# Optimization experiments

Measured on AMD Instinct MI355X. Metric: run time of the kernel, lower is better.

The kernel has to match this reference:

```python
import jax, jax.numpy as jnp
import numpy as np
from jax import lax


def _conv1d(x, w, b, stride, pad):
    # x: [N, 1, L], w: [1, 1, K]
    y = lax.conv_general_dilated(x, w, (stride,), [(pad, pad)],
                                 dimension_numbers=('NCH', 'OIH', 'NCH'))
    return y + b[None, :, None]


def _maxpool1d(x, k, stride, pad):
    # torch MaxPool1d semantics: pad with -inf, window max
    return lax.reduce_window(x, -jnp.inf, lax.max,
                             (1, 1, k), (1, 1, stride),
                             ((0, 0), (0, 0), (pad, pad)))


def setup_inputs() -> dict:
    key = jax.random.key(0)
    ks = jax.random.split(key, 14)
    bs, n, T = 64, 1024, 1200
    return {
        'input':   jax.random.normal(ks[0], (bs, n, T), jnp.float32),
        'conv1_w': jax.random.normal(ks[1], (1, 1, 10), jnp.float32) * 0.3,
        'conv1_b': jax.random.normal(ks[2], (1,), jnp.float32) * 0.1,
        'conv2_w': jax.random.normal(ks[3], (1, 1, 3), jnp.float32) * 0.5,
        'conv2_b': jax.random.normal(ks[4], (1,), jnp.float32) * 0.1,
        'conv3_w': jax.random.normal(ks[5], (1, 1, 4), jnp.float32) * 0.5,
        'conv3_b': jax.random.normal(ks[6], (1,), jnp.float32) * 0.1,
        'gcn1_w':  jax.random.normal(ks[7], (30, 30), jnp.float32) * 0.18,
        'gcn1_b':  jax.random.normal(ks[8], (30,), jnp.float32) * 0.1,
        'gcn2_w':  jax.random.normal(ks[9], (4, 4), jnp.float32) * 0.5,
        'gcn2_b':  jax.random.normal(ks[10], (4,), jnp.float32) * 0.1,
        'cls_w':   jax.random.normal(ks[11], (3, n), jnp.float32) * 0.03,
        'cls_b':   jax.random.normal(ks[12], (3,), jnp.float32) * 0.1,
    }


def reference(input, conv1_w, conv1_b, conv2_w, conv2_b, conv3_w, conv3_b,
              gcn1_w, gcn1_b, gcn2_w, gcn2_b, cls_w, cls_b):
    bs, n, T = input.shape
    # Per-node 1-channel conv chain: fold nodes into the batch dim (replaces
    # the original Python loop over num_nodes issuing tiny Conv1d launches).
    x = input.reshape(bs * n, 1, T)
    h = jax.nn.relu(_conv1d(x, conv1_w, conv1_b, 8, 1))   # L: 1200 -> 150
    h = jax.nn.relu(_maxpool1d(h, 5, 5, 0))               # 150 -> 30
    # NOTE: original applies gcn1 to t_layer_out[2] here, but overwrites an
    # already-consumed list entry -> output is DEAD w.r.t. the final result.
    # (GCNConv over the all-ones adjacency == mean over nodes @ W.T + b.)
    h = jax.nn.relu(_conv1d(h, conv2_w, conv2_b, 3, 0))   # 30 -> 10
    h = jax.nn.relu(_maxpool1d(h, 3, 3, 1))               # 10 -> 4
    # Same dead-code situation for gcn2 on t_layer_out[4].
    h = jax.nn.relu(_conv1d(h, conv3_w, conv3_b, 1, 0))   # 4 -> 1
    feat = h.reshape(bs, n)                               # L5 == 1
    logits = feat @ cls_w.T + cls_b
    return jax.nn.softmax(logits, axis=1)
```

## Files before the change

kernel.cpp:

```cpp
#include <hip/hip_runtime.h>


#define NROWS 65536
#define P1_STRIDE 32

__global__ __launch_bounds__(256, 3) void conv1_pool1_kernel(
    const float* __restrict__ input,
    const float* __restrict__ w1g, const float* __restrict__ b1g,
    float* __restrict__ p1out)
{
    const int t = blockIdx.x * 256 + threadIdx.x;
    const int row = t / 3;
    const int s = t - row * 3;
    const float* rowp = input + (size_t)row * 1200 + s * 400;
    const float4* rp4 = (const float4*)rowp;

    float w1[10];
    #pragma unroll
    for (int k = 0; k < 10; ++k) w1[k] = w1g[k];
    const float b1 = b1g[0];

    float carry = (s == 0) ? 0.0f : rowp[-1];

    float4 cur[10], nxt[10];
    #pragma unroll
    for (int q = 0; q < 10; ++q) cur[q] = rp4[q];

    float* out = p1out + (size_t)row * P1_STRIDE + s * 10;

    #pragma unroll 1
    for (int w = 0; w < 10; ++w) {
        float la;
        if (w < 9) {
            #pragma unroll
            for (int q = 0; q < 10; ++q) nxt[q] = rp4[(w + 1) * 10 + q];
            la = nxt[0].x;
        } else {
            la = (s < 2) ? rowp[400] : 0.0f;
        }

        const float* f = (const float*)cur;
        float pmax = 0.0f;
        #pragma unroll
        for (int i = 0; i < 5; ++i) {
            const float x_m1 = (i == 0) ? carry : f[8 * i - 1];
            const float x_p8 = (i == 4) ? la : f[8 * i + 8];
            float acc = b1;
            acc = fmaf(w1[0], x_m1, acc);
            #pragma unroll
            for (int k = 1; k <= 8; ++k) acc = fmaf(w1[k], f[8 * i - 1 + k], acc);
            acc = fmaf(w1[9], x_p8, acc);
            pmax = fmaxf(pmax, acc);
        }
        out[w] = pmax;

        carry = f[39];
        #pragma unroll
        for (int q = 0; q < 10; ++q) cur[q] = nxt[q];
    }
}

__global__ __launch_bounds__(256) void tail_kernel(
    const float* __restrict__ p1,
    const float* __restrict__ w2g, const float* __restrict__ b2g,
    const float* __restrict__ w3g, const float* __restrict__ b3g,
    float* __restrict__ feat)
{
    const int row = blockIdx.x * 256 + threadIdx.x;
    const float* p = p1 + (size_t)row * P1_STRIDE;

    const float w2a = w2g[0], w2b = w2g[1], w2c = w2g[2];
    const float b2 = b2g[0];

    float y2[10];
    #pragma unroll
    for (int j = 0; j < 10; ++j) {
        float acc = b2;
        acc = fmaf(w2a, p[3 * j], acc);
        acc = fmaf(w2b, p[3 * j + 1], acc);
        acc = fmaf(w2c, p[3 * j + 2], acc);
        y2[j] = fmaxf(acc, 0.0f);
    }
    const float q0 = fmaxf(y2[0], y2[1]);
    const float q1 = fmaxf(fmaxf(y2[2], y2[3]), y2[4]);
    const float q2 = fmaxf(fmaxf(y2[5], y2[6]), y2[7]);
    const float q3 = fmaxf(y2[8], y2[9]);

    float f = b3g[0];
    f = fmaf(w3g[0], q0, f);
    f = fmaf(w3g[1], q1, f);
    f = fmaf(w3g[2], q2, f);
    f = fmaf(w3g[3], q3, f);
    feat[row] = fmaxf(f, 0.0f);
}

__global__ __launch_bounds__(256) void classifier_kernel(
    const float* __restrict__ feat,
    const float* __restrict__ cls_w,
    const float* __restrict__ cls_b,
    float* __restrict__ out)
{
    const int b = blockIdx.x;
    const int tid = threadIdx.x;

    float s0 = 0.0f, s1 = 0.0f, s2 = 0.0f;
    for (int n = tid; n < 1024; n += 256) {
        const float f = feat[b * 1024 + n];
        s0 = fmaf(f, cls_w[n], s0);
        s1 = fmaf(f, cls_w[1024 + n], s1);
        s2 = fmaf(f, cls_w[2048 + n], s2);
    }
    #pragma unroll
    for (int off = 32; off > 0; off >>= 1) {
        s0 += __shfl_down(s0, off, 64);
        s1 += __shfl_down(s1, off, 64);
        s2 += __shfl_down(s2, off, 64);
    }
    __shared__ float red[3][4];
    const int wave = tid >> 6;
    if ((tid & 63) == 0) {
        red[0][wave] = s0;
        red[1][wave] = s1;
        red[2][wave] = s2;
    }
    __syncthreads();
    if (tid == 0) {
        const float l0 = red[0][0] + red[0][1] + red[0][2] + red[0][3] + cls_b[0];
        const float l1 = red[1][0] + red[1][1] + red[1][2] + red[1][3] + cls_b[1];
        const float l2 = red[2][0] + red[2][1] + red[2][2] + red[2][3] + cls_b[2];
        const float m = fmaxf(l0, fmaxf(l1, l2));
        const float e0 = expf(l0 - m);
        const float e1 = expf(l1 - m);
        const float e2 = expf(l2 - m);
        const float inv = 1.0f / (e0 + e1 + e2);
        out[b * 3 + 0] = e0 * inv;
        out[b * 3 + 1] = e1 * inv;
        out[b * 3 + 2] = e2 * inv;
    }
}

extern "C" void kernel_launch(void* const* d_in, const int* in_sizes, int n_in,
                              void* d_out, int out_size, void* d_ws, size_t ws_size,
                              hipStream_t stream) {
    const float* input   = (const float*)d_in[0];
    const float* conv1_w = (const float*)d_in[1];
    const float* conv1_b = (const float*)d_in[2];
    const float* conv2_w = (const float*)d_in[3];
    const float* conv2_b = (const float*)d_in[4];
    const float* conv3_w = (const float*)d_in[5];
    const float* conv3_b = (const float*)d_in[6];
    const float* cls_w   = (const float*)d_in[11];
    const float* cls_b   = (const float*)d_in[12];

    float* wsf  = (float*)d_ws;
    float* feat = wsf;
    float* p1   = wsf + NROWS;
    float* out  = (float*)d_out;

    conv1_pool1_kernel<<<(NROWS * 3) / 256, 256, 0, stream>>>(
        input, conv1_w, conv1_b, p1);
    tail_kernel<<<NROWS / 256, 256, 0, stream>>>(
        p1, conv2_w, conv2_b, conv3_w, conv3_b, feat);
    classifier_kernel<<<64, 256, 0, stream>>>(feat, cls_w, cls_b, out);
}
```

Baseline: 463.7 us.

## Fuse conv chain and classifier partials into one LDS-staged kernel

Replaces the three-kernel pipeline with a single kernel. Each block stages 8 input rows into shared memory with coalesced float4 loads, computes conv1+pool per 40-sample window in 240 threads, then runs the conv2/pool/conv3 tail and the per-node classifier products for 8 rows, writing three partial sums per block. A small second kernel reduces the 128 partials per batch and applies softmax. This removes the intermediate p1/feat global round trips and one launch. In exchange, only 240 of 256 threads work in the conv phase and 8 threads in the tail, and it adds block barriers plus about 39KB of shared memory per block, which may limit occupancy.

```diff
diff --git a/kernel.cpp b/kernel.cpp
--- a/kernel.cpp
+++ b/kernel.cpp
@@ -1,133 +1,130 @@
 #include <hip/hip_runtime.h>
 
 
-#define NROWS 65536
-#define P1_STRIDE 32
+#define ROWS_PER_BLOCK 8
+#define STRIDE_F 1220
+#define STRIDE_F4 305
+#define NBLOCKS 8192
 
-__global__ __launch_bounds__(256, 3) void conv1_pool1_kernel(
+__global__ __launch_bounds__(256) void fused_chain_kernel(
     const float* __restrict__ input,
     const float* __restrict__ w1g, const float* __restrict__ b1g,
-    float* __restrict__ p1out)
+    const float* __restrict__ w2g, const float* __restrict__ b2g,
+    const float* __restrict__ w3g, const float* __restrict__ b3g,
+    const float* __restrict__ cls_w,
+    float* __restrict__ partials)
 {
-    const int t = blockIdx.x * 256 + threadIdx.x;
-    const int row = t / 3;
-    const int s = t - row * 3;
-    const float* rowp = input + (size_t)row * 1200 + s * 400;
-    const float4* rp4 = (const float4*)rowp;
+    __shared__ __align__(16) float xs[ROWS_PER_BLOCK * STRIDE_F];
+    __shared__ float p1s[ROWS_PER_BLOCK][30];
+    __shared__ float pl[ROWS_PER_BLOCK][3];
+
+    const int tid = threadIdx.x;
+    const int blk = blockIdx.x;
+
+    const float4* src = (const float4*)(input + (size_t)blk * 9600);
+    #pragma unroll
+    for (int it = 0; it < 10; ++it) {
+        const int i = tid + it * 256;
+        if (i < 2400) {
+            const float4 vv = src[i];
+            const int r = i / 300;
+            const int c4 = i - r * 300;
+            ((float4*)xs)[r * STRIDE_F4 + c4] = vv;
+        }
+    }
 
     float w1[10];
     #pragma unroll
     for (int k = 0; k < 10; ++k) w1[k] = w1g[k];
     const float b1 = b1g[0];
 
-    float carry = (s == 0) ? 0.0f : rowp[-1];
+    __syncthreads();
 
-    float4 cur[10], nxt[10];
-    #pragma unroll
-    for (int q = 0; q < 10; ++q) cur[q] = rp4[q];
+    if (tid < 240) {
+        const int r = tid & 7;
+        const int w = tid >> 3;
+        const float* xr = xs + r * STRIDE_F + w * 40;
+        float v[42];
+        v[0] = (w == 0) ? 0.0f : xr[-1];
+        #pragma unroll
+        for (int m = 1; m <= 40; ++m) v[m] = xr[m - 1];
+        v[41] = (w == 29) ? 0.0f : xr[40];
 
-    float* out = p1out + (size_t)row * P1_STRIDE + s * 10;
-
-    #pragma unroll 1
-    for (int w = 0; w < 10; ++w) {
-        float la;
-        if (w < 9) {
-            #pragma unroll
-            for (int q = 0; q < 10; ++q) nxt[q] = rp4[(w + 1) * 10 + q];
-            la = nxt[0].x;
-        } else {
-            la = (s < 2) ? rowp[400] : 0.0f;
-        }
-
-        const float* f = (const float*)cur;
         float pmax = 0.0f;
         #pragma unroll
         for (int i = 0; i < 5; ++i) {
-            const float x_m1 = (i == 0) ? carry : f[8 * i - 1];
-            const float x_p8 = (i == 4) ? la : f[8 * i + 8];
             float acc = b1;
-            acc = fmaf(w1[0], x_m1, acc);
             #pragma unroll
-            for (int k = 1; k <= 8; ++k) acc = fmaf(w1[k], f[8 * i - 1 + k], acc);
-            acc = fmaf(w1[9], x_p8, acc);
+            for (int k = 0; k < 10; ++k) acc = fmaf(w1[k], v[8 * i + k], acc);
             pmax = fmaxf(pmax, acc);
         }
-        out[w] = pmax;
+        p1s[r][w] = pmax;
+    }
+    __syncthreads();
 
-        carry = f[39];
+    if (tid < 8) {
+        const float* p = p1s[tid];
+        const float w2a = w2g[0], w2b = w2g[1], w2c = w2g[2], b2 = b2g[0];
+        float y2[10];
         #pragma unroll
-        for (int q = 0; q < 10; ++q) cur[q] = nxt[q];
+        for (int j = 0; j < 10; ++j) {
+            float acc = fmaf(w2c, p[3 * j + 2],
+                        fmaf(w2b, p[3 * j + 1],
+                        fmaf(w2a, p[3 * j], b2)));
+            y2[j] = fmaxf(acc, 0.0f);
+        }
+        const float q0 = fmaxf(y2[0], y2[1]);
+        const float q1 = fmaxf(fmaxf(y2[2], y2[3]), y2[4]);
+        const float q2 = fmaxf(fmaxf(y2[5], y2[6]), y2[7]);
+        const float q3 = fmaxf(y2[8], y2[9]);
+        float f = b3g[0];
+        f = fmaf(w3g[0], q0, f);
+        f = fmaf(w3g[1], q1, f);
+        f = fmaf(w3g[2], q2, f);
+        f = fmaf(w3g[3], q3, f);
+        f = fmaxf(f, 0.0f);
+        const int n = ((blk & 127) << 3) + tid;
+        pl[tid][0] = f * cls_w[n];
+        pl[tid][1] = f * cls_w[1024 + n];
+        pl[tid][2] = f * cls_w[2048 + n];
+    }
+    __syncthreads();
+
+    if (tid < 3) {
+        float s = 0.0f;
+        #pragma unroll
+        for (int r = 0; r < 8; ++r) s += pl[r][tid];
+        partials[blk * 3 + tid] = s;
     }
 }
 
-__global__ __launch_bounds__(256) void tail_kernel(
-    const float* __restrict__ p1,
-    const float* __restrict__ w2g, const float* __restrict__ b2g,
-    const float* __restrict__ w3g, const float* __restrict__ b3g,
-    float* __restrict__ feat)
-{
-    const int row = blockIdx.x * 256 + threadIdx.x;
-    const float* p = p1 + (size_t)row * P1_STRIDE;
-
-    const float w2a = w2g[0], w2b = w2g[1], w2c = w2g[2];
-    const float b2 = b2g[0];
-
-    float y2[10];
-    #pragma unroll
-    for (int j = 0; j < 10; ++j) {
-        float acc = b2;
-        acc = fmaf(w2a, p[3 * j], acc);
-        acc = fmaf(w2b, p[3 * j + 1], acc);
-        acc = fmaf(w2c, p[3 * j + 2], acc);
-        y2[j] = fmaxf(acc, 0.0f);
-    }
-    const float q0 = fmaxf(y2[0], y2[1]);
-    const float q1 = fmaxf(fmaxf(y2[2], y2[3]), y2[4]);
-    const float q2 = fmaxf(fmaxf(y2[5], y2[6]), y2[7]);
-    const float q3 = fmaxf(y2[8], y2[9]);
-
-    float f = b3g[0];
-    f = fmaf(w3g[0], q0, f);
-    f = fmaf(w3g[1], q1, f);
-    f = fmaf(w3g[2], q2, f);
-    f = fmaf(w3g[3], q3, f);
-    feat[row] = fmaxf(f, 0.0f);
-}
-
-__global__ __launch_bounds__(256) void classifier_kernel(
-    const float* __restrict__ feat,
-    const float* __restrict__ cls_w,
+__global__ __launch_bounds__(128) void reduce_softmax_kernel(
+    const float* __restrict__ partials,
     const float* __restrict__ cls_b,
     float* __restrict__ out)
 {
     const int b = blockIdx.x;
-    const int tid = threadIdx.x;
-
-    float s0 = 0.0f, s1 = 0.0f, s2 = 0.0f;
-    for (int n = tid; n < 1024; n += 256) {
-        const float f = feat[b * 1024 + n];
-        s0 = fmaf(f, cls_w[n], s0);
-        s1 = fmaf(f, cls_w[1024 + n], s1);
-        s2 = fmaf(f, cls_w[2048 + n], s2);
-    }
+    const int t = threadIdx.x;
+    const float* p = partials + (size_t)b * 128 * 3 + t * 3;
+    float s0 = p[0], s1 = p[1], s2 = p[2];
     #pragma unroll
     for (int off = 32; off > 0; off >>= 1) {
         s0 += __shfl_down(s0, off, 64);
         s1 += __shfl_down(s1, off, 64);
         s2 += __shfl_down(s2, off, 64);
     }
-    __shared__ float red[3][4];
-    const int wave = tid >> 6;
-    if ((tid & 63) == 0) {
-        red[0][wave] = s0;
-        red[1][wave] = s1;
-        red[2][wave] = s2;
+    __shared__ float red[3][2];
+    if ((t & 63) == 0) {
+        const int w = t >> 6;
+        red[0][w] = s0;
+        red[1][w] = s1;
+        red[2][w] = s2;
     }
     __syncthreads();
-    if (tid == 0) {
-        const float l0 = red[0][0] + red[0][1] + red[0][2] + red[0][3] + cls_b[0];
-        const float l1 = red[1][0] + red[1][1] + red[1][2] + red[1][3] + cls_b[1];
-        const float l2 = red[2][0] + red[2][1] + red[2][2] + red[2][3] + cls_b[2];
+    if (t == 0) {
+        const float l0 = red[0][0] + red[0][1] + cls_b[0];
+        const float l1 = red[1][0] + red[1][1] + cls_b[1];
+        const float l2 = red[2][0] + red[2][1] + cls_b[2];
         const float m = fmaxf(l0, fmaxf(l1, l2));
         const float e0 = expf(l0 - m);
         const float e1 = expf(l1 - m);
@@ -152,14 +149,11 @@
     const float* cls_w   = (const float*)d_in[11];
     const float* cls_b   = (const float*)d_in[12];
 
-    float* wsf  = (float*)d_ws;
-    float* feat = wsf;
-    float* p1   = wsf + NROWS;
-    float* out  = (float*)d_out;
+    float* partials = (float*)d_ws;
+    float* out      = (float*)d_out;
 
-    conv1_pool1_kernel<<<(NROWS * 3) / 256, 256, 0, stream>>>(
-        input, conv1_w, conv1_b, p1);
-    tail_kernel<<<NROWS / 256, 256, 0, stream>>>(
-        p1, conv2_w, conv2_b, conv3_w, conv3_b, feat);
-    classifier_kernel<<<64, 256, 0, stream>>>(feat, cls_w, cls_b, out);
+    fused_chain_kernel<<<NBLOCKS, 256, 0, stream>>>(
+        input, conv1_w, conv1_b, conv2_w, conv2_b, conv3_w, conv3_b,
+        cls_w, partials);
+    reduce_softmax_kernel<<<64, 128, 0, stream>>>(partials, cls_b, out);
 }
```

Result: faster. 424.6 us (-8.4%).

## Fuse conv1/pool1 with tail via LDS-staged rows and wave shuffles

Applied to the files above, without the earlier changes.

Replaces the per-thread streaming conv1+pool1 kernel and the separate tail kernel with one kernel. Each 128-thread block loads 4 full rows into padded LDS with coalesced float4 loads. Each of 30 lanes per half-wave then computes one pool1 output, and conv2, pool2 and conv3 run through wave shuffles. This drops the p1 intermediate round trip and one launch, at the cost of LDS use (about 19.5KB per block), idle lanes, and a sync per block.

```diff
diff --git a/kernel.cpp b/kernel.cpp
--- a/kernel.cpp
+++ b/kernel.cpp
@@ -2,96 +2,95 @@
 
 
 #define NROWS 65536
-#define P1_STRIDE 32
+#define ROWS_PER_BLOCK 4
+#define STRIDE_F 1220
+#define STRIDE_F4 305
+#define NBLOCKS (NROWS / ROWS_PER_BLOCK)
 
-__global__ __launch_bounds__(256, 3) void conv1_pool1_kernel(
+__global__ __launch_bounds__(128, 4) void fused_chain_kernel(
     const float* __restrict__ input,
     const float* __restrict__ w1g, const float* __restrict__ b1g,
-    float* __restrict__ p1out)
+    const float* __restrict__ w2g, const float* __restrict__ b2g,
+    const float* __restrict__ w3g, const float* __restrict__ b3g,
+    float* __restrict__ feat)
 {
-    const int t = blockIdx.x * 256 + threadIdx.x;
-    const int row = t / 3;
-    const int s = t - row * 3;
-    const float* rowp = input + (size_t)row * 1200 + s * 400;
-    const float4* rp4 = (const float4*)rowp;
+    __shared__ __align__(16) float xs[ROWS_PER_BLOCK * STRIDE_F];
+
+    const int tid = threadIdx.x;
+    const int blk = blockIdx.x;
+
+    const float4* src = (const float4*)(input + (size_t)blk * 4800);
+    #pragma unroll
+    for (int it = 0; it < 10; ++it) {
+        const int i = tid + it * 128;
+        if (i < 1200) {
+            const float4 vv = src[i];
+            const int r = i / 300;
+            const int c4 = i - r * 300;
+            ((float4*)xs)[r * STRIDE_F4 + c4] = vv;
+        }
+    }
 
     float w1[10];
     #pragma unroll
     for (int k = 0; k < 10; ++k) w1[k] = w1g[k];
     const float b1 = b1g[0];
 
-    float carry = (s == 0) ? 0.0f : rowp[-1];
+    __syncthreads();
 
-    float4 cur[10], nxt[10];
-    #pragma unroll
-    for (int q = 0; q < 10; ++q) cur[q] = rp4[q];
+    const int lane = tid & 63;
+    const int wave = tid >> 6;
+    const int half = lane >> 5;
+    const int w = lane & 31;
+    const int rib = wave * 2 + half;
 
-    float* out = p1out + (size_t)row * P1_STRIDE + s * 10;
+    const float* xr = xs + rib * STRIDE_F + w * 40;
+    float pmax = 0.0f;
+    if (w < 30) {
+        float v[42];
+        v[0] = (w == 0) ? 0.0f : xr[-1];
+        #pragma unroll
+        for (int m = 1; m <= 40; ++m) v[m] = xr[m - 1];
+        v[41] = (w == 29) ? 0.0f : xr[40];
 
-    #pragma unroll 1
-    for (int w = 0; w < 10; ++w) {
-        float la;
-        if (w < 9) {
-            #pragma unroll
-            for (int q = 0; q < 10; ++q) nxt[q] = rp4[(w + 1) * 10 + q];
-            la = nxt[0].x;
-        } else {
-            la = (s < 2) ? rowp[400] : 0.0f;
-        }
-
-        const float* f = (const float*)cur;
-        float pmax = 0.0f;
         #pragma unroll
         for (int i = 0; i < 5; ++i) {
-            const float x_m1 = (i == 0) ? carry : f[8 * i - 1];
-            const float x_p8 = (i == 4) ? la : f[8 * i + 8];
             float acc = b1;
-            acc = fmaf(w1[0], x_m1, acc);
             #pragma unroll
-            for (int k = 1; k <= 8; ++k) acc = fmaf(w1[k], f[8 * i - 1 + k], acc);
-            acc = fmaf(w1[9], x_p8, acc);
+            for (int k = 0; k < 10; ++k) acc = fmaf(w1[k], v[8 * i + k], acc);
             pmax = fmaxf(pmax, acc);
         }
-        out[w] = pmax;
+    }
 
-        carry = f[39];
-        #pragma unroll
-        for (int q = 0; q < 10; ++q) cur[q] = nxt[q];
+    const int base = lane & 32;
+    const int jj = (w < 10) ? w : 9;
+    const float pa = __shfl(pmax, base + 3 * jj, 64);
+    const float pb = __shfl(pmax, base + 3 * jj + 1, 64);
+    const float pc = __shfl(pmax, base + 3 * jj + 2, 64);
+    const float w2a = w2g[0], w2b = w2g[1], w2c = w2g[2];
+    const float y2 = fmaxf(fmaf(w2c, pc, fmaf(w2b, pb, fmaf(w2a, pa, b2g[0]))), 0.0f);
+
+    const float t1 = __shfl(y2, base + 1, 64);
+    const float t2 = __shfl(y2, base + 2, 64);
+    const float t3 = __shfl(y2, base + 3, 64);
+    const float t4 = __shfl(y2, base + 4, 64);
+    const float t5 = __shfl(y2, base + 5, 64);
+    const float t6 = __shfl(y2, base + 6, 64);
+    const float t7 = __shfl(y2, base + 7, 64);
+    const float t8 = __shfl(y2, base + 8, 64);
+    const float t9 = __shfl(y2, base + 9, 64);
+    if (w == 0) {
+        const float q0 = fmaxf(y2, t1);
+        const float q1 = fmaxf(fmaxf(t2, t3), t4);
+        const float q2 = fmaxf(fmaxf(t5, t6), t7);
+        const float q3 = fmaxf(t8, t9);
+        float f = b3g[0];
+        f = fmaf(w3g[0], q0, f);
+        f = fmaf(w3g[1], q1, f);
+        f = fmaf(w3g[2], q2, f);
+        f = fmaf(w3g[3], q3, f);
+        feat[(size_t)blk * ROWS_PER_BLOCK + rib] = fmaxf(f, 0.0f);
     }
-}
-
-__global__ __launch_bounds__(256) void tail_kernel(
-    const float* __restrict__ p1,
-    const float* __restrict__ w2g, const float* __restrict__ b2g,
-    const float* __restrict__ w3g, const float* __restrict__ b3g,
-    float* __restrict__ feat)
-{
-    const int row = blockIdx.x * 256 + threadIdx.x;
-    const float* p = p1 + (size_t)row * P1_STRIDE;
-
-    const float w2a = w2g[0], w2b = w2g[1], w2c = w2g[2];
-    const float b2 = b2g[0];
-
-    float y2[10];
-    #pragma unroll
-    for (int j = 0; j < 10; ++j) {
-        float acc = b2;
-        acc = fmaf(w2a, p[3 * j], acc);
-        acc = fmaf(w2b, p[3 * j + 1], acc);
-        acc = fmaf(w2c, p[3 * j + 2], acc);
-        y2[j] = fmaxf(acc, 0.0f);
-    }
-    const float q0 = fmaxf(y2[0], y2[1]);
-    const float q1 = fmaxf(fmaxf(y2[2], y2[3]), y2[4]);
-    const float q2 = fmaxf(fmaxf(y2[5], y2[6]), y2[7]);
-    const float q3 = fmaxf(y2[8], y2[9]);
-
-    float f = b3g[0];
-    f = fmaf(w3g[0], q0, f);
-    f = fmaf(w3g[1], q1, f);
-    f = fmaf(w3g[2], q2, f);
-    f = fmaf(w3g[3], q3, f);
-    feat[row] = fmaxf(f, 0.0f);
 }
 
 __global__ __launch_bounds__(256) void classifier_kernel(
@@ -152,14 +151,10 @@
     const float* cls_w   = (const float*)d_in[11];
     const float* cls_b   = (const float*)d_in[12];
 
-    float* wsf  = (float*)d_ws;
-    float* feat = wsf;
-    float* p1   = wsf + NROWS;
-    float* out  = (float*)d_out;
+    float* featbuf = (float*)d_ws;
+    float* out     = (float*)d_out;
 
-    conv1_pool1_kernel<<<(NROWS * 3) / 256, 256, 0, stream>>>(
-        input, conv1_w, conv1_b, p1);
-    tail_kernel<<<NROWS / 256, 256, 0, stream>>>(
-        p1, conv2_w, conv2_b, conv3_w, conv3_b, feat);
-    classifier_kernel<<<64, 256, 0, stream>>>(feat, cls_w, cls_b, out);
+    fused_chain_kernel<<<NBLOCKS, 128, 0, stream>>>(
+        input, conv1_w, conv1_b, conv2_w, conv2_b, conv3_w, conv3_b, featbuf);
+    classifier_kernel<<<64, 256, 0, stream>>>(featbuf, cls_w, cls_b, out);
 }
```

New measurement: 433.8 us. 6.5% less time.
